# Optimization experiments

Measured on AMD Instinct MI355X. Metric: run time of the kernel, lower is better.

## Reference

```python
import jax, jax.numpy as jnp
import numpy as np

NUM_NODES = 50000
NUM_EDGES = 1600000
IN_DIM = 128
OUT_DIM = 128
BATCH = 2


def setup_inputs() -> dict:
    key = jax.random.key(0)
    k1, k2, k3 = jax.random.split(key, 3)
    inputs = jax.random.normal(k1, (BATCH, NUM_NODES, IN_DIM), dtype=jnp.float32)
    W = jax.random.normal(k2, (IN_DIM, OUT_DIM), dtype=jnp.float32) * 0.02
    bias = jnp.zeros((1, 1, OUT_DIM), dtype=jnp.float32)
    adjacency_list = jax.random.randint(k3, (NUM_EDGES, 2), 0, NUM_NODES, dtype=jnp.int32)
    return {"inputs": inputs, "W": W, "bias": bias, "adjacency_list": adjacency_list}


def reference(inputs, W, bias, adjacency_list):
    # inputs: (B, N, Din); adjacency_list: (E, 2) with [:,0]=src, [:,1]=dst
    N = inputs.shape[1]
    src = adjacency_list[:, 0]
    dst = adjacency_list[:, 1]
    # symmetric-normalization weights, as computed in __init__
    deg = jnp.bincount(src, length=N)                      # (N,)
    node_w = jnp.sqrt(1.0 / (deg.astype(inputs.dtype) + 1.0))  # (N,)
    edge_w = node_w[src] * node_w[dst]                     # (E,)
    # dense projection (no activation: activation=None)
    x = jnp.einsum('bnd,do->bno', inputs, W)               # (B, N, Dout)
    # gather by edge source, scale by edge weight
    gathered = x[:, src, :] * edge_w[None, :, None]        # (B, E, Dout)
    # scatter-add into destination nodes (unsorted_segment_sum)
    agg = jnp.zeros_like(x).at[:, dst, :].add(gathered)    # (B, N, Dout)
    # self-loop term + aggregated neighbors + bias
    out = (node_w ** 2)[None, :, None] * x + agg + bias
    return out
```

## Files before the change

kernel.cpp:

```cpp
#include <hip/hip_runtime.h>
#include <hip/hip_bf16.h>


#define NN 50000
#define EE 1600000
#define DD 128
#define BB 2
#define NB 128
#define CHUNK 12500
#define HS 50000
#define HW4 (HS / 4)

typedef __attribute__((ext_vector_type(8))) short short8;
typedef __attribute__((ext_vector_type(8))) unsigned short ushort8v;
typedef __attribute__((ext_vector_type(4))) float floatx4;

__device__ inline unsigned short f2bf(float f) {
    unsigned u = __float_as_uint(f);
    unsigned r = u + 0x7fffu + ((u >> 16) & 1u);
    return (unsigned short)(r >> 16);
}
__device__ inline float bf2f(unsigned short h) {
    return __uint_as_float(((unsigned)h) << 16);
}

__global__ __launch_bounds__(1024) void phist_kernel(const int4* __restrict__ adj2,
                                                     unsigned int* __restrict__ histD32,
                                                     unsigned int* __restrict__ histS32,
                                                     unsigned char* __restrict__ rank) {
    __shared__ unsigned int h[HW4];
    int b = blockIdx.x;
    int p0 = b * (CHUNK / 2);

    for (int i = threadIdx.x; i < HW4; i += 1024) h[i] = 0;
    __syncthreads();
    if (blockIdx.y == 0) {
        for (int i = threadIdx.x; i < CHUNK / 2; i += 1024) {
            int4 two = adj2[p0 + i];
            unsigned ka = (unsigned)two.y, kb = (unsigned)two.w;
            unsigned sha = (ka & 3u) << 3, shb = (kb & 3u) << 3;
            unsigned olda = atomicAdd(&h[ka >> 2], 1u << sha);
            unsigned oldb = atomicAdd(&h[kb >> 2], 1u << shb);
            unsigned r0 = (olda >> sha) & 0xffu;
            unsigned r1 = (oldb >> shb) & 0xffu;
            int e = b * CHUNK + 2 * i;
            *(unsigned short*)(rank + e) = (unsigned short)(r0 | (r1 << 8));
        }
        __syncthreads();
        for (int i = threadIdx.x; i < HW4; i += 1024) histD32[(size_t)b * HW4 + i] = h[i];
    } else {
        for (int i = threadIdx.x; i < CHUNK / 2; i += 1024) {
            int4 two = adj2[p0 + i];
            unsigned ka = (unsigned)two.x, kb = (unsigned)two.z;
            atomicAdd(&h[ka >> 2], 1u << ((ka & 3u) << 3));
            atomicAdd(&h[kb >> 2], 1u << ((kb & 3u) << 3));
        }
        __syncthreads();
        for (int i = threadIdx.x; i < HW4; i += 1024) histS32[(size_t)b * HW4 + i] = h[i];
    }
}

__global__ __launch_bounds__(256) void reduce_hist_kernel(unsigned char* __restrict__ histD,
                                                          const unsigned char* __restrict__ histS,
                                                          unsigned char* __restrict__ deg8,
                                                          float* __restrict__ node_w,
                                                          int* __restrict__ blocksum) {
    int k = blockIdx.x * 256 + threadIdx.x;
    unsigned run = 0;
    if (k < NN) {
#pragma unroll 4
        for (int b = 0; b < NB; ++b) {
            size_t idx = (size_t)b * HS + k;
            unsigned c = histD[idx];
            histD[idx] = (unsigned char)run;
            run += c;
        }
        deg8[k] = (unsigned char)run;

        unsigned s = 0;
#pragma unroll 8
        for (int b = 0; b < NB; ++b) s += histS[(size_t)b * HS + k];
        node_w[k] = rsqrtf((float)s + 1.0f);
    }
    __shared__ int red[256];
    red[threadIdx.x] = (int)run;
    __syncthreads();
    for (int s2 = 128; s2 > 0; s2 >>= 1) {
        if (threadIdx.x < s2) red[threadIdx.x] += red[threadIdx.x + s2];
        __syncthreads();
    }
    if (threadIdx.x == 0) blocksum[blockIdx.x] = red[0];
}

__global__ __launch_bounds__(256) void offsets_kernel(const unsigned char* __restrict__ deg8,
                                                      const int* __restrict__ blocksum,
                                                      int* __restrict__ offsets) {
    __shared__ int base_s;
    __shared__ int s[256];
    int bid = blockIdx.x;
    if (threadIdx.x < 64) {
        int v = 0;
        for (int i = threadIdx.x; i < bid; i += 64) v += blocksum[i];
#pragma unroll
        for (int o = 32; o > 0; o >>= 1) v += __shfl_down(v, o);
        if (threadIdx.x == 0) base_s = v;
    }
    int t = bid * 256 + threadIdx.x;
    int d = (t < NN) ? deg8[t] : 0;
    s[threadIdx.x] = d;
    __syncthreads();
    for (int off = 1; off < 256; off <<= 1) {
        int v = (threadIdx.x >= off) ? s[threadIdx.x - off] : 0;
        __syncthreads();
        s[threadIdx.x] += v;
        __syncthreads();
    }
    if (t < NN) offsets[t] = base_s + s[threadIdx.x] - d;
}

__global__ __launch_bounds__(256) void scatter_kernel(const int4* __restrict__ adj2,
                                                      const unsigned short* __restrict__ rank16,
                                                      const unsigned char* __restrict__ histD,
                                                      const int* __restrict__ offsets,
                                                      unsigned short* __restrict__ csr_src) {
    int i = blockIdx.x * blockDim.x + threadIdx.x;
    int4 two = adj2[i];
    unsigned rr = rank16[i];
    int e = 2 * i;
    int b = e / CHUNK;
    int posA = offsets[two.y] + (int)histD[(size_t)b * HS + two.y] + (int)(rr & 0xffu);
    int posB = offsets[two.w] + (int)histD[(size_t)b * HS + two.w] + (int)(rr >> 8);
    csr_src[posA] = (unsigned short)two.x;
    csr_src[posB] = (unsigned short)two.z;
}

__global__ __launch_bounds__(256) void sort_csr_kernel(unsigned short* __restrict__ csr_src,
                                                       const int* __restrict__ offsets,
                                                       const unsigned char* __restrict__ deg8) {
    int wave = threadIdx.x >> 6;
    int lane = threadIdx.x & 63;
    int n = blockIdx.x * 4 + wave;
    int start = offsets[n];
    int cnt = deg8[n];
    for (int base = 0; base < cnt; base += 64) {
        int mm = cnt - base; if (mm > 64) mm = 64;
        int v = (lane < mm) ? (int)csr_src[start + base + lane] : 0x7fffffff;
#pragma unroll
        for (int k = 2; k <= 64; k <<= 1) {
#pragma unroll
            for (int j = k >> 1; j > 0; j >>= 1) {
                int other = __shfl_xor(v, j);
                bool lower = (lane & j) == 0;
                bool up = (lane & k) == 0;
                int mn = other < v ? other : v;
                int mx = other < v ? v : other;
                v = up ? (lower ? mn : mx) : (lower ? mx : mn);
            }
        }
        if (lane < mm) csr_src[start + base + lane] = (unsigned short)v;
    }
}

#define WT_STRIDE 136
__global__ __launch_bounds__(1024) void gemm_mfma_kernel(const float* __restrict__ in,
                                                         const float* __restrict__ W,
                                                         const float* __restrict__ node_w,
                                                         unsigned short* __restrict__ y,
                                                         int total_rows) {
    __shared__ unsigned short wt[128 * WT_STRIDE];
    for (int i = threadIdx.x; i < 128 * 128; i += 1024) {
        int d = i >> 7, o = i & 127;
        wt[o * WT_STRIDE + d] = f2bf(W[i]);
    }
    __syncthreads();

    int wave = threadIdx.x >> 6;
    int lane = threadIdx.x & 63;
    int m = lane & 15;
    int quad = lane >> 4;
    int rt = (blockIdx.x * 16 + wave) * 16;
    if (rt >= total_rows) return;

    short8 a[4];
    const float* arow = in + (size_t)(rt + m) * 128;
#pragma unroll
    for (int kt = 0; kt < 4; ++kt) {
        int k0 = kt * 32 + quad * 8;
        float4 f0 = *(const float4*)(arow + k0);
        float4 f1 = *(const float4*)(arow + k0 + 4);
        short8 av;
        av[0] = (short)f2bf(f0.x); av[1] = (short)f2bf(f0.y);
        av[2] = (short)f2bf(f0.z); av[3] = (short)f2bf(f0.w);
        av[4] = (short)f2bf(f1.x); av[5] = (short)f2bf(f1.y);
        av[6] = (short)f2bf(f1.z); av[7] = (short)f2bf(f1.w);
        a[kt] = av;
    }

    float nw[4];
#pragma unroll
    for (int r = 0; r < 4; ++r) {
        int row = rt + quad * 4 + r;
        int n = row - (row >= NN ? NN : 0);
        nw[r] = node_w[n];
    }

#pragma unroll
    for (int ct = 0; ct < 8; ++ct) {
        floatx4 acc = {0.f, 0.f, 0.f, 0.f};
#pragma unroll
        for (int kt = 0; kt < 4; ++kt) {
            const short8* bp =
                (const short8*)&wt[(ct * 16 + m) * WT_STRIDE + kt * 32 + quad * 8];
            acc = __builtin_amdgcn_mfma_f32_16x16x32_bf16(a[kt], *bp, acc, 0, 0, 0);
        }
        int col = ct * 16 + m;
#pragma unroll
        for (int r = 0; r < 4; ++r) {
            int row = rt + quad * 4 + r;
            y[(size_t)row * 128 + col] = f2bf(nw[r] * acc[r]);
        }
    }
}

__global__ __launch_bounds__(256) void aggregate_kernel(
    const unsigned short* __restrict__ yb, const unsigned short* __restrict__ csr_src,
    const int* __restrict__ offsets, const unsigned char* __restrict__ deg8,
    const float* __restrict__ node_w, const float* __restrict__ bias,
    float* __restrict__ out) {
    int wave = threadIdx.x >> 6;
    int lane = threadIdx.x & 63;
    unsigned blk = blockIdx.x;
    int xcd = (int)(blk & 7u);
    int bg = xcd >> 2;
    int nbid = (int)(blk >> 3) * 4 + (xcd & 3);
    int n = nbid * 4 + wave;

    int g = lane >> 4;
    int c8 = lane & 15;
    int c16 = c8 * 16;
    const char* ybase = (const char*)yb + (size_t)bg * (NN * 128 * 2);

    int start = offsets[n];
    int cnt = deg8[n];

    float acc[8];
#pragma unroll
    for (int k = 0; k < 8; ++k) acc[k] = 0.f;

    for (int base = 0; base < cnt; base += 64) {
        int mm = cnt - base; if (mm > 64) mm = 64;
        int sv = ((int)csr_src[start + base + lane]) << 8;
        int j = 0;
        for (; j + 32 <= mm; j += 32) {
            int o0 = __shfl(sv, j + g) + c16;
            int o1 = __shfl(sv, j + 4 + g) + c16;
            int o2 = __shfl(sv, j + 8 + g) + c16;
            int o3 = __shfl(sv, j + 12 + g) + c16;
            int o4 = __shfl(sv, j + 16 + g) + c16;
            int o5 = __shfl(sv, j + 20 + g) + c16;
            int o6 = __shfl(sv, j + 24 + g) + c16;
            int o7 = __shfl(sv, j + 28 + g) + c16;
            ushort8v ld0 = *(const ushort8v*)(ybase + (unsigned)o0);
            ushort8v ld1 = *(const ushort8v*)(ybase + (unsigned)o1);
            ushort8v ld2 = *(const ushort8v*)(ybase + (unsigned)o2);
            ushort8v ld3 = *(const ushort8v*)(ybase + (unsigned)o3);
            ushort8v ld4 = *(const ushort8v*)(ybase + (unsigned)o4);
            ushort8v ld5 = *(const ushort8v*)(ybase + (unsigned)o5);
            ushort8v ld6 = *(const ushort8v*)(ybase + (unsigned)o6);
            ushort8v ld7 = *(const ushort8v*)(ybase + (unsigned)o7);
#pragma unroll
            for (int k = 0; k < 8; ++k) acc[k] += bf2f((unsigned short)ld0[k]);
#pragma unroll
            for (int k = 0; k < 8; ++k) acc[k] += bf2f((unsigned short)ld1[k]);
#pragma unroll
            for (int k = 0; k < 8; ++k) acc[k] += bf2f((unsigned short)ld2[k]);
#pragma unroll
            for (int k = 0; k < 8; ++k) acc[k] += bf2f((unsigned short)ld3[k]);
#pragma unroll
            for (int k = 0; k < 8; ++k) acc[k] += bf2f((unsigned short)ld4[k]);
#pragma unroll
            for (int k = 0; k < 8; ++k) acc[k] += bf2f((unsigned short)ld5[k]);
#pragma unroll
            for (int k = 0; k < 8; ++k) acc[k] += bf2f((unsigned short)ld6[k]);
#pragma unroll
            for (int k = 0; k < 8; ++k) acc[k] += bf2f((unsigned short)ld7[k]);
        }
        for (; j + 16 <= mm; j += 16) {
            int o0 = __shfl(sv, j + g) + c16;
            int o1 = __shfl(sv, j + 4 + g) + c16;
            int o2 = __shfl(sv, j + 8 + g) + c16;
            int o3 = __shfl(sv, j + 12 + g) + c16;
            ushort8v ld0 = *(const ushort8v*)(ybase + (unsigned)o0);
            ushort8v ld1 = *(const ushort8v*)(ybase + (unsigned)o1);
            ushort8v ld2 = *(const ushort8v*)(ybase + (unsigned)o2);
            ushort8v ld3 = *(const ushort8v*)(ybase + (unsigned)o3);
#pragma unroll
            for (int k = 0; k < 8; ++k) acc[k] += bf2f((unsigned short)ld0[k]);
#pragma unroll
            for (int k = 0; k < 8; ++k) acc[k] += bf2f((unsigned short)ld1[k]);
#pragma unroll
            for (int k = 0; k < 8; ++k) acc[k] += bf2f((unsigned short)ld2[k]);
#pragma unroll
            for (int k = 0; k < 8; ++k) acc[k] += bf2f((unsigned short)ld3[k]);
        }
        for (; j + 8 <= mm; j += 8) {
            int o0 = __shfl(sv, j + g) + c16;
            int o1 = __shfl(sv, j + 4 + g) + c16;
            ushort8v ld0 = *(const ushort8v*)(ybase + (unsigned)o0);
            ushort8v ld1 = *(const ushort8v*)(ybase + (unsigned)o1);
#pragma unroll
            for (int k = 0; k < 8; ++k) acc[k] += bf2f((unsigned short)ld0[k]);
#pragma unroll
            for (int k = 0; k < 8; ++k) acc[k] += bf2f((unsigned short)ld1[k]);
        }
        if (j < mm) {
            int i0 = j + g, i1 = j + 4 + g;
            int o0 = __shfl(sv, i0 < mm ? i0 : 0) + c16;
            int o1 = __shfl(sv, i1 < mm ? i1 : 0) + c16;
            if (i0 < mm) {
                ushort8v ld0 = *(const ushort8v*)(ybase + (unsigned)o0);
#pragma unroll
                for (int k = 0; k < 8; ++k) acc[k] += bf2f((unsigned short)ld0[k]);
            }
            if (i1 < mm) {
                ushort8v ld1 = *(const ushort8v*)(ybase + (unsigned)o1);
#pragma unroll
                for (int k = 0; k < 8; ++k) acc[k] += bf2f((unsigned short)ld1[k]);
            }
        }
    }

#pragma unroll
    for (int k = 0; k < 8; ++k) {
        acc[k] += __shfl_xor(acc[k], 16);
        acc[k] += __shfl_xor(acc[k], 32);
    }

    if (g == 0) {
        float nw = node_w[n];
        const unsigned short* ys = yb + (size_t)bg * (NN * 128) + (size_t)n * 128 + c8 * 8;
        ushort8v yv = *(const ushort8v*)ys;
        floatx4 o0, o1;
        const float* bp = bias + c8 * 8;
        o0.x = nw * (acc[0] + bf2f((unsigned short)yv[0])) + bp[0];
        o0.y = nw * (acc[1] + bf2f((unsigned short)yv[1])) + bp[1];
        o0.z = nw * (acc[2] + bf2f((unsigned short)yv[2])) + bp[2];
        o0.w = nw * (acc[3] + bf2f((unsigned short)yv[3])) + bp[3];
        o1.x = nw * (acc[4] + bf2f((unsigned short)yv[4])) + bp[4];
        o1.y = nw * (acc[5] + bf2f((unsigned short)yv[5])) + bp[5];
        o1.z = nw * (acc[6] + bf2f((unsigned short)yv[6])) + bp[6];
        o1.w = nw * (acc[7] + bf2f((unsigned short)yv[7])) + bp[7];
        float* op = out + ((size_t)bg * NN + n) * 128 + c8 * 8;
        __builtin_nontemporal_store(o0, (floatx4*)op);
        __builtin_nontemporal_store(o1, (floatx4*)(op + 4));
    }
}

extern "C" void kernel_launch(void* const* d_in, const int* in_sizes, int n_in,
                              void* d_out, int out_size, void* d_ws, size_t ws_size,
                              hipStream_t stream) {
    const float* inputs = (const float*)d_in[0];
    const float* W      = (const float*)d_in[1];
    const float* bias   = (const float*)d_in[2];
    const int*   adj    = (const int*)d_in[3];
    float* out = (float*)d_out;

    const int total_rows = BB * NN;

    char* ws = (char*)d_ws;
    size_t off = 0;
    unsigned short* y = (unsigned short*)(ws + off);
    off += (size_t)BB * NN * DD * sizeof(unsigned short);
    unsigned char* histD = (unsigned char*)(ws + off);
    off += (size_t)NB * HS;
    unsigned char* histS = (unsigned char*)(ws + off);
    off += (size_t)NB * HS;
    unsigned short* csr_src = (unsigned short*)histS;
    unsigned char* rank = (unsigned char*)(ws + off);
    off += (size_t)EE;
    unsigned char* deg8 = (unsigned char*)(ws + off);
    off += (size_t)((NN + 255) & ~255);
    float* node_w = (float*)(ws + off);  off += (size_t)NN * sizeof(float);
    int* offsets = (int*)(ws + off);     off += (size_t)NN * sizeof(int);
    int* blocksum = (int*)(ws + off);    off += 256 * sizeof(int);

    dim3 hgrid(NB, 2);
    phist_kernel<<<hgrid, 1024, 0, stream>>>((const int4*)adj, (unsigned int*)histD,
                                             (unsigned int*)histS, rank);
    reduce_hist_kernel<<<(NN + 255) / 256, 256, 0, stream>>>(histD, histS, deg8, node_w,
                                                             blocksum);
    offsets_kernel<<<(NN + 255) / 256, 256, 0, stream>>>(deg8, blocksum, offsets);
    scatter_kernel<<<EE / 2 / 256, 256, 0, stream>>>((const int4*)adj,
                                                     (const unsigned short*)rank, histD, offsets,
                                                     csr_src);
    sort_csr_kernel<<<NN / 4, 256, 0, stream>>>(csr_src, offsets, deg8);
    gemm_mfma_kernel<<<(total_rows + 255) / 256, 1024, 0, stream>>>(inputs, W, node_w, y,
                                                                    total_rows);
    aggregate_kernel<<<NN / 4 * BB, 256, 0, stream>>>(y, csr_src, offsets, deg8, node_w, bias,
                                                      out);
}
```

Measured before the change: 281.4 us.

## Fuse per-node CSR bitonic sort into aggregate kernel and drop sort launch

Removes the separate sort_csr_kernel and performs the wave-level bitonic sort of each node's neighbor list inside aggregate_kernel before gathering. This saves one kernel launch plus a read-modify-write pass over csr_src. The cost is that the sort now runs once per batch (twice per node), and the 32-wide unrolled gather loop is removed, leaving the 16-wide loop. The reduce_hist unroll is also raised from 4 to 8.

New measurement: 265.5 us. 1.06x faster.

```diff
diff --git a/kernel.cpp b/kernel.cpp
--- a/kernel.cpp
+++ b/kernel.cpp
@@ -68,7 +68,7 @@
     int k = blockIdx.x * 256 + threadIdx.x;
     unsigned run = 0;
     if (k < NN) {
-#pragma unroll 4
+#pragma unroll 8
         for (int b = 0; b < NB; ++b) {
             size_t idx = (size_t)b * HS + k;
             unsigned c = histD[idx];
@@ -134,33 +134,6 @@
     csr_src[posB] = (unsigned short)two.z;
 }
 
-__global__ __launch_bounds__(256) void sort_csr_kernel(unsigned short* __restrict__ csr_src,
-                                                       const int* __restrict__ offsets,
-                                                       const unsigned char* __restrict__ deg8) {
-    int wave = threadIdx.x >> 6;
-    int lane = threadIdx.x & 63;
-    int n = blockIdx.x * 4 + wave;
-    int start = offsets[n];
-    int cnt = deg8[n];
-    for (int base = 0; base < cnt; base += 64) {
-        int mm = cnt - base; if (mm > 64) mm = 64;
-        int v = (lane < mm) ? (int)csr_src[start + base + lane] : 0x7fffffff;
-#pragma unroll
-        for (int k = 2; k <= 64; k <<= 1) {
-#pragma unroll
-            for (int j = k >> 1; j > 0; j >>= 1) {
-                int other = __shfl_xor(v, j);
-                bool lower = (lane & j) == 0;
-                bool up = (lane & k) == 0;
-                int mn = other < v ? other : v;
-                int mx = other < v ? v : other;
-                v = up ? (lower ? mn : mx) : (lower ? mx : mn);
-            }
-        }
-        if (lane < mm) csr_src[start + base + lane] = (unsigned short)v;
-    }
-}
-
 #define WT_STRIDE 136
 __global__ __launch_bounds__(1024) void gemm_mfma_kernel(const float* __restrict__ in,
                                                          const float* __restrict__ W,
@@ -249,42 +222,21 @@
 
     for (int base = 0; base < cnt; base += 64) {
         int mm = cnt - base; if (mm > 64) mm = 64;
-        int sv = ((int)csr_src[start + base + lane]) << 8;
+        int v = (lane < mm) ? (int)csr_src[start + base + lane] : 0x7fffffff;
+#pragma unroll
+        for (int k = 2; k <= 64; k <<= 1) {
+#pragma unroll
+            for (int j = k >> 1; j > 0; j >>= 1) {
+                int other = __shfl_xor(v, j);
+                bool lower = (lane & j) == 0;
+                bool up = (lane & k) == 0;
+                int mn = other < v ? other : v;
+                int mx = other < v ? v : other;
+                v = up ? (lower ? mn : mx) : (lower ? mx : mn);
+            }
+        }
+        int sv = v << 8;
         int j = 0;
-        for (; j + 32 <= mm; j += 32) {
-            int o0 = __shfl(sv, j + g) + c16;
-            int o1 = __shfl(sv, j + 4 + g) + c16;
-            int o2 = __shfl(sv, j + 8 + g) + c16;
-            int o3 = __shfl(sv, j + 12 + g) + c16;
-            int o4 = __shfl(sv, j + 16 + g) + c16;
-            int o5 = __shfl(sv, j + 20 + g) + c16;
-            int o6 = __shfl(sv, j + 24 + g) + c16;
-            int o7 = __shfl(sv, j + 28 + g) + c16;
-            ushort8v ld0 = *(const ushort8v*)(ybase + (unsigned)o0);
-            ushort8v ld1 = *(const ushort8v*)(ybase + (unsigned)o1);
-            ushort8v ld2 = *(const ushort8v*)(ybase + (unsigned)o2);
-            ushort8v ld3 = *(const ushort8v*)(ybase + (unsigned)o3);
-            ushort8v ld4 = *(const ushort8v*)(ybase + (unsigned)o4);
-            ushort8v ld5 = *(const ushort8v*)(ybase + (unsigned)o5);
-            ushort8v ld6 = *(const ushort8v*)(ybase + (unsigned)o6);
-            ushort8v ld7 = *(const ushort8v*)(ybase + (unsigned)o7);
-#pragma unroll
-            for (int k = 0; k < 8; ++k) acc[k] += bf2f((unsigned short)ld0[k]);
-#pragma unroll
-            for (int k = 0; k < 8; ++k) acc[k] += bf2f((unsigned short)ld1[k]);
-#pragma unroll
-            for (int k = 0; k < 8; ++k) acc[k] += bf2f((unsigned short)ld2[k]);
-#pragma unroll
-            for (int k = 0; k < 8; ++k) acc[k] += bf2f((unsigned short)ld3[k]);
-#pragma unroll
-            for (int k = 0; k < 8; ++k) acc[k] += bf2f((unsigned short)ld4[k]);
-#pragma unroll
-            for (int k = 0; k < 8; ++k) acc[k] += bf2f((unsigned short)ld5[k]);
-#pragma unroll
-            for (int k = 0; k < 8; ++k) acc[k] += bf2f((unsigned short)ld6[k]);
-#pragma unroll
-            for (int k = 0; k < 8; ++k) acc[k] += bf2f((unsigned short)ld7[k]);
-        }
         for (; j + 16 <= mm; j += 16) {
             int o0 = __shfl(sv, j + g) + c16;
             int o1 = __shfl(sv, j + 4 + g) + c16;
@@ -393,7 +345,6 @@
     scatter_kernel<<<EE / 2 / 256, 256, 0, stream>>>((const int4*)adj,
                                                      (const unsigned short*)rank, histD, offsets,
                                                      csr_src);
-    sort_csr_kernel<<<NN / 4, 256, 0, stream>>>(csr_src, offsets, deg8);
     gemm_mfma_kernel<<<(total_rows + 255) / 256, 1024, 0, stream>>>(inputs, W, node_w, y,
                                                                     total_rows);
     aggregate_kernel<<<NN / 4 * BB, 256, 0, stream>>>(y, csr_src, offsets, deg8, node_w, bias,
```
